# Optimization experiments

Measured on AMD Instinct MI355X. Metric: run time of the kernel, lower is better.

The kernel has to match this reference:

```python
import jax, jax.numpy as jnp
import numpy as np

B, S, D = 4, 1024, 1024
H, DK, DV = 16, 64, 64


def setup_inputs() -> dict:
    key = jax.random.key(0)
    ks = jax.random.split(key, 8)
    sc = 0.02
    return {
        "queries": jax.random.normal(ks[0], (B, S, D), jnp.float32),
        "keys": jax.random.normal(ks[1], (B, S, D), jnp.float32),
        "values": jax.random.normal(ks[2], (B, S, D), jnp.float32),
        "attn_bias": jax.random.normal(ks[3], (B, 1, S, S), jnp.float32),
        "Wq": jax.random.normal(ks[4], (H * DK, D), jnp.float32) * sc,
        "Wk": jax.random.normal(ks[5], (H * DK, D), jnp.float32) * sc,
        "Wv": jax.random.normal(ks[6], (H * DV, D), jnp.float32) * sc,
        "Wp": jax.random.normal(ks[7], (D, H * DV), jnp.float32) * sc,
    }


def reference(queries, keys, values, attn_bias, Wq, Wk, Wv, Wp):
    # Linear (no bias): x @ W.T, then split heads -> [B, H, S, d]
    q = (queries @ Wq.T).reshape(B, S, H, DK).transpose(0, 2, 1, 3)
    k = (keys @ Wk.T).reshape(B, S, H, DK).transpose(0, 2, 1, 3)
    v = (values @ Wv.T).reshape(B, S, H, DV).transpose(0, 2, 1, 3)
    # NOTE: original scales by d_model**-0.5, not d_key**-0.5
    scores = jnp.einsum("bhqd,bhkd->bhqk", q, k) * (D ** -0.5)
    scores = scores + attn_bias  # bias broadcasts over heads
    weights = jax.nn.softmax(scores, axis=-1)
    out = jnp.einsum("bhqk,bhkd->bhqd", weights, v)  # [B,H,S,DV]
    out = out.transpose(0, 2, 1, 3).reshape(B, S, H * DV)
    return out @ Wp.T
```

## Files before the change

### kernel.cpp

```cpp
#include <hip/hip_runtime.h>
#include <hip/hip_bf16.h>

typedef unsigned short u16;
typedef unsigned int u32;
typedef __attribute__((ext_vector_type(8))) short bf16x8;
typedef __attribute__((ext_vector_type(8))) u16 u16x8;
typedef __attribute__((ext_vector_type(4))) u16 u16x4;
typedef __attribute__((ext_vector_type(2))) u32 u32x2;
typedef __attribute__((ext_vector_type(4))) u32 u32x4;
typedef __attribute__((ext_vector_type(4))) float f32x4;
typedef __attribute__((ext_vector_type(4))) _Float16 f16x4;
typedef __attribute__((ext_vector_type(8))) _Float16 f16x8;
typedef __attribute__((ext_vector_type(16))) float f32x16;

typedef const __attribute__((address_space(1))) void* gas1_t;
typedef __attribute__((address_space(3))) void* las3_t;

#define MFMA16(a,b,c) __builtin_amdgcn_mfma_f32_16x16x32_bf16((a),(b),(c),0,0,0)
#define MFMA32(a,b,c) __builtin_amdgcn_mfma_f32_32x32x16_bf16((a),(b),(c),0,0,0)

static constexpr int BB = 4, SS = 1024, DD = 1024, HH = 16;

static __device__ __forceinline__ u16 f2b(float x) {
  union { __hip_bfloat16 h; u16 u; } cv;
  cv.h = __float2bfloat16(x);
  return cv.u;
}
static __device__ __forceinline__ u32 pk2(float a, float b) {
  return (u32)f2b(a) | ((u32)f2b(b) << 16);
}
static __device__ __forceinline__ u32 cvtpk(float lo, float hi) {
  u32 r;
  asm("v_cvt_pk_bf16_f32 %0, %1, %2" : "=v"(r) : "v"(lo), "v"(hi));
  return r;
}

__global__ __launch_bounds__(256) void cvt_all(
    const float* __restrict__ wq_, const float* __restrict__ wk_, const float* __restrict__ wv_,
    const float* __restrict__ wp_, const float* __restrict__ bias,
    u16* __restrict__ wqb, u16* __restrict__ wkb, u16* __restrict__ wvb, u16* __restrict__ wpb,
    _Float16* __restrict__ bias16) {
  int bid = blockIdx.x;
  if (bid >= 4096) {
    int G = (bid - 4096) * 256 + threadIdx.x;
    int gi = G & 1023;
    int ctid = gi & 255, g = gi >> 8;
    int T = G >> 10;
    int kt = T & 15, qt = (T >> 4) & 7, b_ = T >> 7;
    int wq = ctid >> 6, hi = (ctid >> 5) & 1, ln = ctid & 31;
    int qrow = qt * 128 + wq * 32 + ln;
    int kbf = g >> 1, j = g & 1;
    int k0 = kt * 64 + kbf * 32 + j * 16 + hi * 4;
    const float* src = bias + (((size_t)(b_ * 1024 + qrow)) << 10) + k0;
    float4 lo = *(const float4*)(src);
    float4 up = *(const float4*)(src + 8);
    f16x8 r = { (_Float16)lo.x, (_Float16)lo.y, (_Float16)lo.z, (_Float16)lo.w,
                (_Float16)up.x, (_Float16)up.y, (_Float16)up.z, (_Float16)up.w };
    *(f16x8*)(bias16 + (((size_t)T) << 13) + g * 2048 + ctid * 8) = r;
    return;
  }
  const float* s; u16* d; int off;
  if      (bid < 1024) { s = wq_; d = wqb; off = bid; }
  else if (bid < 2048) { s = wk_; d = wkb; off = bid - 1024; }
  else if (bid < 3072) { s = wv_; d = wvb; off = bid - 2048; }
  else                 { s = wp_; d = wpb; off = bid - 3072; }
  int i = (off * 256 + threadIdx.x) * 4;
  float4 val = *(const float4*)(s + i);
  u16x4 r = { f2b(val.x), f2b(val.y), f2b(val.z), f2b(val.w) };
  *(u16x4*)(d + i) = r;
}

__global__ __launch_bounds__(512) void gemm_qkv(
    const float* __restrict__ Qf, const float* __restrict__ Kf, const float* __restrict__ Vf,
    const u16* __restrict__ Wbase, u16* __restrict__ Qb, u16* __restrict__ Kb,
    u16* __restrict__ Vtb) {
  const int z = blockIdx.z;
  const float* A = z == 0 ? Qf : (z == 1 ? Kf : Vf);
  const u16* W = Wbase + (size_t)z * (DD * DD);

  __shared__ __align__(16) u16 As[128 * 64];
  __shared__ __align__(16) u16 Bs[128 * 64];

  const int tid = threadIdx.x;
  const int lane = tid & 63;
  const int wid = tid >> 6;
  const int g = lane >> 4;
  const int li = lane & 15;

  const int hw = blockIdx.x + (blockIdx.y << 3);
  const int L = ((hw & 7) << 5) + (hw >> 3);
  const int brow = (L >> 3) * 128;
  const int bcol = (L & 7) * 128;

  const int wr = (wid >> 1) * 32;
  const int wc = (wid & 1) * 64;

  const int arow = tid >> 4;
  const int ag = tid & 15;
  const float* ga0 = A + (size_t)(brow + arow) * DD + ag * 4;
  const u32 awb = (u32)((((ag >> 1) ^ (arow & 7)) << 4) + ((ag & 1) << 3));

  const int srw = tid >> 3;
  const int spw = (tid & 7) ^ (srw & 7);
  const u16* gw0 = W + (size_t)(bcol + srw) * DD + spw * 8;

  f32x4 acc[2][4] = {};

  f32x4 ar0 = *(const f32x4*)(ga0 + (size_t)(0 * 32) * DD);
  f32x4 ar1 = *(const f32x4*)(ga0 + (size_t)(1 * 32) * DD);
  f32x4 ar2 = *(const f32x4*)(ga0 + (size_t)(2 * 32) * DD);
  f32x4 ar3 = *(const f32x4*)(ga0 + (size_t)(3 * 32) * DD);

  for (int k0 = 0; k0 < DD; k0 += 64) {
#pragma unroll
    for (int i = 0; i < 2; ++i)
      __builtin_amdgcn_global_load_lds((gas1_t)(const void*)(gw0 + (size_t)(i * 64) * DD + k0),
                                       (las3_t)(void*)(Bs + (i * 64 + (wid << 3)) * 64), 16, 0, 0);
    {
      u32x2 w0 = { cvtpk(ar0[0], ar0[1]), cvtpk(ar0[2], ar0[3]) };
      u32x2 w1 = { cvtpk(ar1[0], ar1[1]), cvtpk(ar1[2], ar1[3]) };
      u32x2 w2 = { cvtpk(ar2[0], ar2[1]), cvtpk(ar2[2], ar2[3]) };
      u32x2 w3 = { cvtpk(ar3[0], ar3[1]), cvtpk(ar3[2], ar3[3]) };
      char* ab = (char*)As + arow * 128 + awb;
      *(u32x2*)(ab + 0 * 32 * 128) = w0;
      *(u32x2*)(ab + 1 * 32 * 128) = w1;
      *(u32x2*)(ab + 2 * 32 * 128) = w2;
      *(u32x2*)(ab + 3 * 32 * 128) = w3;
    }
    if (k0 < DD - 64) {
      ar0 = *(const f32x4*)(ga0 + (size_t)(0 * 32) * DD + k0 + 64);
      ar1 = *(const f32x4*)(ga0 + (size_t)(1 * 32) * DD + k0 + 64);
      ar2 = *(const f32x4*)(ga0 + (size_t)(2 * 32) * DD + k0 + 64);
      ar3 = *(const f32x4*)(ga0 + (size_t)(3 * 32) * DD + k0 + 64);
    }
    __syncthreads();

#pragma unroll
    for (int kk = 0; kk < 2; ++kk) {
      bf16x8 a[2], b[4];
#pragma unroll
      for (int m = 0; m < 2; ++m) {
        int row = wr + m * 16 + li;
        a[m] = *(const bf16x8*)&As[row * 64 + (((kk * 4 + g) ^ (li & 7)) << 3)];
      }
#pragma unroll
      for (int n = 0; n < 4; ++n) {
        int row = wc + n * 16 + li;
        b[n] = *(const bf16x8*)&Bs[row * 64 + (((kk * 4 + g) ^ (li & 7)) << 3)];
      }
#pragma unroll
      for (int m = 0; m < 2; ++m)
#pragma unroll
        for (int n = 0; n < 4; ++n)
          acc[m][n] = MFMA16(a[m], b[n], acc[m][n]);
    }
    __syncthreads();
  }

  if (z == 2) {
#pragma unroll
    for (int m = 0; m < 2; ++m) {
#pragma unroll
      for (int n = 0; n < 4; ++n) {
        int c = bcol + wc + n * 16 + li;
        int h_ = c >> 6, dv = c & 63;
        int r0 = brow + wr + m * 16 + g * 4;
        int b_ = r0 >> 10, s0 = r0 & 1023;
        u16x4 val = { f2b(acc[m][n][0]), f2b(acc[m][n][1]),
                      f2b(acc[m][n][2]), f2b(acc[m][n][3]) };
        *(u16x4*)&Vtb[(size_t)((b_ * HH + h_) * 64 + dv) * SS + s0] = val;
      }
    }
  } else {
    u16* C = z == 0 ? Qb : Kb;
#pragma unroll
    for (int m = 0; m < 2; ++m)
#pragma unroll
      for (int n = 0; n < 4; ++n)
#pragma unroll
        for (int j = 0; j < 4; ++j) {
          int r = brow + wr + m * 16 + g * 4 + j;
          int c = bcol + wc + n * 16 + li;
          C[(size_t)r * DD + c] = f2b(acc[m][n][j]);
        }
  }
}

__global__ __launch_bounds__(512) void gemm_proj(
    const u16* __restrict__ A, const u16* __restrict__ W, float* __restrict__ C,
    int N, int K) {
  __shared__ __align__(16) u16 As[128 * 64];
  __shared__ __align__(16) u16 Bs[128 * 64];

  const int tid = threadIdx.x;
  const int lane = tid & 63;
  const int wid = tid >> 6;
  const int g = lane >> 4;
  const int li = lane & 15;

  const int hw = blockIdx.x + (blockIdx.y << 3);
  const int L = ((hw & 7) << 5) + (hw >> 3);
  const int brow = (L >> 3) * 128;
  const int bcol = (L & 7) * 128;

  const int wr = (wid >> 1) * 32;
  const int wc = (wid & 1) * 64;

  const int srow = tid >> 3;
  const int schunk = (tid & 7) ^ (srow & 7);
  const u16* ga0 = A + (size_t)(brow + srow) * K + schunk * 8;
  const u16* gw0 = W + (size_t)(bcol + srow) * K + schunk * 8;

  f32x4 acc[2][4] = {};

  for (int k0 = 0; k0 < K; k0 += 64) {
#pragma unroll
    for (int i = 0; i < 2; ++i) {
      __builtin_amdgcn_global_load_lds((gas1_t)(const void*)(ga0 + (size_t)(i * 64) * K + k0),
                                       (las3_t)(void*)(As + (i * 64 + (wid << 3)) * 64), 16, 0, 0);
      __builtin_amdgcn_global_load_lds((gas1_t)(const void*)(gw0 + (size_t)(i * 64) * K + k0),
                                       (las3_t)(void*)(Bs + (i * 64 + (wid << 3)) * 64), 16, 0, 0);
    }
    __syncthreads();

#pragma unroll
    for (int kk = 0; kk < 2; ++kk) {
      bf16x8 a[2], b[4];
#pragma unroll
      for (int m = 0; m < 2; ++m) {
        int row = wr + m * 16 + li;
        a[m] = *(const bf16x8*)&As[row * 64 + (((kk * 4 + g) ^ (li & 7)) << 3)];
      }
#pragma unroll
      for (int n = 0; n < 4; ++n) {
        int row = wc + n * 16 + li;
        b[n] = *(const bf16x8*)&Bs[row * 64 + (((kk * 4 + g) ^ (li & 7)) << 3)];
      }
#pragma unroll
      for (int m = 0; m < 2; ++m)
#pragma unroll
        for (int n = 0; n < 4; ++n)
          acc[m][n] = MFMA16(a[m], b[n], acc[m][n]);
    }
    __syncthreads();
  }

#pragma unroll
  for (int m = 0; m < 2; ++m)
#pragma unroll
    for (int n = 0; n < 4; ++n)
#pragma unroll
      for (int j = 0; j < 4; ++j) {
        int r = brow + wr + m * 16 + g * 4 + j;
        int c = bcol + wc + n * 16 + li;
        C[(size_t)r * N + c] = acc[m][n][j];
      }
}

__global__ __launch_bounds__(256) void attn_kernel(
    const u16* __restrict__ Q, const u16* __restrict__ K, const u16* __restrict__ Vt,
    const _Float16* __restrict__ bias16, u16* __restrict__ O) {
  __shared__ __align__(16) u16 kbuf[2][64 * 64];
  __shared__ __align__(16) u16 vbuf[2][64 * 64];

  const int tid = threadIdx.x;
  const int lane = tid & 63;
  const int wq = tid >> 6;
  const int hi = lane >> 5;
  const int ln = lane & 31;
  const u32 swz = (u32)(ln & 7) << 4;

  const int flat = blockIdx.x + (blockIdx.y << 3) + (blockIdx.z << 7);
  const int L = ((flat & 7) << 6) | (flat >> 3);
  const int qt = L & 7, h = (L >> 3) & 15, b = L >> 7;
  const int q0 = qt * 128;
  const int qrow = q0 + wq * 32 + ln;

  bf16x8 qf[4];
  {
    const u16* qp = Q + (size_t)(b * SS + qrow) * DD + h * 64 + hi * 8;
#pragma unroll
    for (int d = 0; d < 4; ++d) qf[d] = *(const bf16x8*)(qp + d * 16);
  }

  const int srow = (lane >> 3);
  const int spc = ((lane & 7) ^ srow) * 8;
  const u16* kgl = K + (size_t)(b * SS + wq * 16 + srow) * DD + h * 64 + spc;
  const u16* vgl = Vt + (size_t)((b * HH + h) * 64 + wq * 16 + srow) * SS + spc;

  const _Float16* btile = bias16 + (((size_t)(b * 8 + qt) * 16) << 13) + tid * 8;

  {
    char* kd = (char*)kbuf[0] + wq * 2048;
    char* vd = (char*)vbuf[0] + wq * 2048;
#pragma unroll
    for (int j = 0; j < 2; ++j) {
      __builtin_amdgcn_global_load_lds((gas1_t)(const void*)(kgl + (size_t)(j * 8) * DD),
                                       (las3_t)(void*)(kd + j * 1024), 16, 0, 0);
      __builtin_amdgcn_global_load_lds((gas1_t)(const void*)(vgl + (size_t)(j * 8) * SS),
                                       (las3_t)(void*)(vd + j * 1024), 16, 0, 0);
    }
  }
  f16x8 bbr[4], bbn[4];
#pragma unroll
  for (int g = 0; g < 4; ++g)
    bbr[g] = *(const f16x8*)(btile + g * 2048);
  __syncthreads();

  f32x16 o0 = {}, o1 = {};
  float m = -1e30f, lsum = 0.f;
  int cur = 0;

  for (int kt = 0; kt < 16; ++kt) {
    if (kt < 15) {
      char* kd = (char*)kbuf[cur ^ 1] + wq * 2048;
      char* vd = (char*)vbuf[cur ^ 1] + wq * 2048;
      const size_t k1 = (size_t)(kt + 1) * 64;
#pragma unroll
      for (int j = 0; j < 2; ++j) {
        __builtin_amdgcn_global_load_lds((gas1_t)(const void*)(kgl + (k1 + j * 8) * DD),
                                         (las3_t)(void*)(kd + j * 1024), 16, 0, 0);
        __builtin_amdgcn_global_load_lds((gas1_t)(const void*)(vgl + (size_t)(j * 8) * SS + k1),
                                         (las3_t)(void*)(vd + j * 1024), 16, 0, 0);
      }
      const _Float16* bt = btile + ((size_t)(kt + 1) << 13);
#pragma unroll
      for (int g = 0; g < 4; ++g)
        bbn[g] = *(const f16x8*)(bt + g * 2048);
    }

    const char* kb_base = (const char*)kbuf[cur];
    f32x16 s[2];
#pragma unroll
    for (int kb = 0; kb < 2; ++kb) {
      f32x16 acc = {};
#pragma unroll
      for (int d = 0; d < 4; ++d) {
        bf16x8 kf = *(const bf16x8*)(kb_base + (kb * 32 + ln) * 128 + (((u32)(d * 32 + hi * 16)) ^ swz));
        acc = MFMA32(kf, qf[d], acc);
      }
      s[kb] = acc;
    }

#pragma unroll
    for (int g = 0; g < 4; ++g) {
      const int kb = g >> 1, rq0 = (g & 1) * 2;
#pragma unroll
      for (int e = 0; e < 8; ++e)
        s[kb][(rq0 + (e >> 2)) * 4 + (e & 3)] =
            fmaf(s[kb][(rq0 + (e >> 2)) * 4 + (e & 3)], 0.03125f, (float)bbr[g][e]);
    }

    float mt = -1e30f;
#pragma unroll
    for (int r = 0; r < 16; ++r) { mt = fmaxf(mt, s[0][r]); mt = fmaxf(mt, s[1][r]); }
    mt = fmaxf(mt, __shfl_xor(mt, 32));

    bool resc = false;
    float fsc = 1.f;
    if (kt == 0) {
      m = mt;
    } else if (__any(mt > m + 8.f)) {
      float mn = fmaxf(m, mt);
      fsc = __expf(m - mn);
      m = mn;
      resc = true;
    }

    float rs = 0.f;
    u32 wv[2][8];
#pragma unroll
    for (int kb = 0; kb < 2; ++kb)
#pragma unroll
      for (int t = 0; t < 8; ++t) {
        float p0 = __expf(s[kb][2 * t] - m);
        float p1 = __expf(s[kb][2 * t + 1] - m);
        rs += p0 + p1;
        wv[kb][t] = pk2(p0, p1);
      }
    rs += __shfl_xor(rs, 32);
    lsum = lsum * fsc + rs;

    if (resc) {
#pragma unroll
      for (int j = 0; j < 16; ++j) {
        float fv = __shfl(fsc, (j & 3) + 8 * (j >> 2) + 4 * hi);
        o0[j] *= fv; o1[j] *= fv;
      }
    }

    const char* vb_base = (const char*)vbuf[cur];
#pragma unroll
    for (int ks = 0; ks < 4; ++ks) {
      const int kb = ks >> 1, i0 = (ks & 1) * 4;
      u32 sA = hi ? wv[kb][i0 + 0] : wv[kb][i0 + 2];
      u32 sB = hi ? wv[kb][i0 + 1] : wv[kb][i0 + 3];
      u32 rA = (u32)__shfl_xor((int)sA, 32);
      u32 rB = (u32)__shfl_xor((int)sB, 32);
      u32 e0 = hi ? rA : wv[kb][i0 + 0];
      u32 e1 = hi ? rB : wv[kb][i0 + 1];
      u32 e2 = hi ? wv[kb][i0 + 2] : rA;
      u32 e3 = hi ? wv[kb][i0 + 3] : rB;
      union { u32x4 u; bf16x8 v; } pc;
      pc.u = (u32x4){e0, e1, e2, e3};
      bf16x8 pa = pc.v;
#pragma unroll
      for (int nv = 0; nv < 2; ++nv) {
        bf16x8 vf = *(const bf16x8*)(vb_base + (nv * 32 + ln) * 128 + (((u32)(ks * 32 + hi * 16)) ^ swz));
        if (nv == 0) o0 = MFMA32(pa, vf, o0);
        else         o1 = MFMA32(pa, vf, o1);
      }
    }

    if (kt < 15) {
      __syncthreads();
      cur ^= 1;
#pragma unroll
      for (int g = 0; g < 4; ++g) bbr[g] = bbn[g];
    }
  }

  float inv = 1.0f / lsum;
#pragma unroll
  for (int j = 0; j < 16; ++j) {
    float iv = __shfl(inv, (j & 3) + 8 * (j >> 2) + 4 * hi);
    int q = q0 + wq * 32 + (j & 3) + 8 * (j >> 2) + 4 * hi;
    u16* op = O + (size_t)(b * SS + q) * DD + h * 64 + ln;
    op[0]  = f2b(o0[j] * iv);
    op[32] = f2b(o1[j] * iv);
  }
}

extern "C" void kernel_launch(void* const* d_in, const int* in_sizes, int n_in,
                              void* d_out, int out_size, void* d_ws, size_t ws_size,
                              hipStream_t stream) {
  const float* queries = (const float*)d_in[0];
  const float* keys    = (const float*)d_in[1];
  const float* values  = (const float*)d_in[2];
  const float* bias    = (const float*)d_in[3];
  const float* Wq      = (const float*)d_in[4];
  const float* Wk      = (const float*)d_in[5];
  const float* Wv      = (const float*)d_in[6];
  const float* Wp      = (const float*)d_in[7];
  float* out = (float*)d_out;

  char* ws = (char*)d_ws;
  const size_t MB = 1024 * 1024;
  u16* wqb = (u16*)(ws + 24 * MB);
  u16* wkb = (u16*)(ws + 26 * MB);
  u16* wvb = (u16*)(ws + 28 * MB);
  u16* wpb = (u16*)(ws + 30 * MB);
  u16* Qb  = (u16*)(ws + 32 * MB);
  u16* Kb  = (u16*)(ws + 40 * MB);
  _Float16* bias16 = (_Float16*)(ws + 48 * MB);
  u16* Vtb = (u16*)(ws + 56 * MB);
  u16* Ob  = (u16*)(ws + 0 * MB);

  cvt_all<<<dim3(6144), dim3(256), 0, stream>>>(
      Wq, Wk, Wv, Wp, bias, wqb, wkb, wvb, wpb, bias16);

  gemm_qkv<<<dim3(8, 32, 3), dim3(512), 0, stream>>>(
      queries, keys, values, wqb, Qb, Kb, Vtb);

  attn_kernel<<<dim3(8, 16, 4), dim3(256), 0, stream>>>(Qb, Kb, Vtb, bias16, Ob);

  gemm_proj<<<dim3(8, 32, 1), dim3(512), 0, stream>>>(Ob, wpb, out, DD, DD);
}
```

Baseline: 112.0 us.

## Double-buffer weight tiles in QKV GEMM to overlap loads with MFMA

Gives the QKV projection GEMM two LDS buffers for the bf16 weight tile. The next tile's global-to-LDS load and the next fp32 activation register load are issued before the current tile's MFMAs run. The activation tile stays single-buffered and is written after a barrier. This aims to hide global load latency behind compute, at the cost of more LDS per block (possible occupancy loss) and an extra barrier per iteration.

```diff
diff --git a/kernel.cpp b/kernel.cpp
--- a/kernel.cpp
+++ b/kernel.cpp
@@ -79,7 +79,7 @@
   const u16* W = Wbase + (size_t)z * (DD * DD);
 
   __shared__ __align__(16) u16 As[128 * 64];
-  __shared__ __align__(16) u16 Bs[128 * 64];
+  __shared__ __align__(16) u16 Bs[2][128 * 64];
 
   const int tid = threadIdx.x;
   const int lane = tid & 63;
@@ -105,35 +105,43 @@
   const u16* gw0 = W + (size_t)(bcol + srw) * DD + spw * 8;
 
   f32x4 acc[2][4] = {};
-
-  f32x4 ar0 = *(const f32x4*)(ga0 + (size_t)(0 * 32) * DD);
-  f32x4 ar1 = *(const f32x4*)(ga0 + (size_t)(1 * 32) * DD);
-  f32x4 ar2 = *(const f32x4*)(ga0 + (size_t)(2 * 32) * DD);
-  f32x4 ar3 = *(const f32x4*)(ga0 + (size_t)(3 * 32) * DD);
-
-  for (int k0 = 0; k0 < DD; k0 += 64) {
-#pragma unroll
-    for (int i = 0; i < 2; ++i)
-      __builtin_amdgcn_global_load_lds((gas1_t)(const void*)(gw0 + (size_t)(i * 64) * DD + k0),
-                                       (las3_t)(void*)(Bs + (i * 64 + (wid << 3)) * 64), 16, 0, 0);
-    {
-      u32x2 w0 = { cvtpk(ar0[0], ar0[1]), cvtpk(ar0[2], ar0[3]) };
-      u32x2 w1 = { cvtpk(ar1[0], ar1[1]), cvtpk(ar1[2], ar1[3]) };
-      u32x2 w2 = { cvtpk(ar2[0], ar2[1]), cvtpk(ar2[2], ar2[3]) };
-      u32x2 w3 = { cvtpk(ar3[0], ar3[1]), cvtpk(ar3[2], ar3[3]) };
-      char* ab = (char*)As + arow * 128 + awb;
-      *(u32x2*)(ab + 0 * 32 * 128) = w0;
-      *(u32x2*)(ab + 1 * 32 * 128) = w1;
-      *(u32x2*)(ab + 2 * 32 * 128) = w2;
-      *(u32x2*)(ab + 3 * 32 * 128) = w3;
-    }
-    if (k0 < DD - 64) {
-      ar0 = *(const f32x4*)(ga0 + (size_t)(0 * 32) * DD + k0 + 64);
-      ar1 = *(const f32x4*)(ga0 + (size_t)(1 * 32) * DD + k0 + 64);
-      ar2 = *(const f32x4*)(ga0 + (size_t)(2 * 32) * DD + k0 + 64);
-      ar3 = *(const f32x4*)(ga0 + (size_t)(3 * 32) * DD + k0 + 64);
-    }
-    __syncthreads();
+  f32x4 ar0, ar1, ar2, ar3;
+
+  ar0 = *(const f32x4*)(ga0 + (size_t)(0 * 32) * DD);
+  ar1 = *(const f32x4*)(ga0 + (size_t)(1 * 32) * DD);
+  ar2 = *(const f32x4*)(ga0 + (size_t)(2 * 32) * DD);
+  ar3 = *(const f32x4*)(ga0 + (size_t)(3 * 32) * DD);
+#pragma unroll
+  for (int i = 0; i < 2; ++i)
+    __builtin_amdgcn_global_load_lds((gas1_t)(const void*)(gw0 + (size_t)(i * 64) * DD),
+                                     (las3_t)(void*)(Bs[0] + (i * 64 + (wid << 3)) * 64), 16, 0, 0);
+  {
+    u32x2 w0 = { cvtpk(ar0[0], ar0[1]), cvtpk(ar0[2], ar0[3]) };
+    u32x2 w1 = { cvtpk(ar1[0], ar1[1]), cvtpk(ar1[2], ar1[3]) };
+    u32x2 w2 = { cvtpk(ar2[0], ar2[1]), cvtpk(ar2[2], ar2[3]) };
+    u32x2 w3 = { cvtpk(ar3[0], ar3[1]), cvtpk(ar3[2], ar3[3]) };
+    char* ab = (char*)As + arow * 128 + awb;
+    *(u32x2*)(ab + 0 * 32 * 128) = w0;
+    *(u32x2*)(ab + 1 * 32 * 128) = w1;
+    *(u32x2*)(ab + 2 * 32 * 128) = w2;
+    *(u32x2*)(ab + 3 * 32 * 128) = w3;
+  }
+  __syncthreads();
+
+  int cur = 0;
+  for (int k = 0; k < 16; ++k) {
+    if (k < 15) {
+      const size_t koff = (size_t)(k + 1) * 64;
+      ar0 = *(const f32x4*)(ga0 + (size_t)(0 * 32) * DD + koff);
+      ar1 = *(const f32x4*)(ga0 + (size_t)(1 * 32) * DD + koff);
+      ar2 = *(const f32x4*)(ga0 + (size_t)(2 * 32) * DD + koff);
+      ar3 = *(const f32x4*)(ga0 + (size_t)(3 * 32) * DD + koff);
+#pragma unroll
+      for (int i = 0; i < 2; ++i)
+        __builtin_amdgcn_global_load_lds(
+            (gas1_t)(const void*)(gw0 + (size_t)(i * 64) * DD + koff),
+            (las3_t)(void*)(Bs[cur ^ 1] + (i * 64 + (wid << 3)) * 64), 16, 0, 0);
+    }
 
 #pragma unroll
     for (int kk = 0; kk < 2; ++kk) {
@@ -146,7 +154,7 @@
 #pragma unroll
       for (int n = 0; n < 4; ++n) {
         int row = wc + n * 16 + li;
-        b[n] = *(const bf16x8*)&Bs[row * 64 + (((kk * 4 + g) ^ (li & 7)) << 3)];
+        b[n] = *(const bf16x8*)&Bs[cur][row * 64 + (((kk * 4 + g) ^ (li & 7)) << 3)];
       }
 #pragma unroll
       for (int m = 0; m < 2; ++m)
@@ -154,7 +162,23 @@
         for (int n = 0; n < 4; ++n)
           acc[m][n] = MFMA16(a[m], b[n], acc[m][n]);
     }
-    __syncthreads();
+
+    if (k < 15) {
+      __syncthreads();
+      {
+        u32x2 w0 = { cvtpk(ar0[0], ar0[1]), cvtpk(ar0[2], ar0[3]) };
+        u32x2 w1 = { cvtpk(ar1[0], ar1[1]), cvtpk(ar1[2], ar1[3]) };
+        u32x2 w2 = { cvtpk(ar2[0], ar2[1]), cvtpk(ar2[2], ar2[3]) };
+        u32x2 w3 = { cvtpk(ar3[0], ar3[1]), cvtpk(ar3[2], ar3[3]) };
+        char* ab = (char*)As + arow * 128 + awb;
+        *(u32x2*)(ab + 0 * 32 * 128) = w0;
+        *(u32x2*)(ab + 1 * 32 * 128) = w1;
+        *(u32x2*)(ab + 2 * 32 * 128) = w2;
+        *(u32x2*)(ab + 3 * 32 * 128) = w3;
+      }
+      __syncthreads();
+      cur ^= 1;
+    }
   }
 
   if (z == 2) {
```

Result: no change. 113.7 us (+1.5%).
